# Kernel optimization log

Hardware: AMD Instinct MI355X
Metric: run time of the kernel (lower is better)

The kernel has to match this reference:

```python
import jax, jax.numpy as jnp
import numpy as np
import math

D_MODEL = 1024
N_HEADS = 16
HEAD_DIM = D_MODEL // N_HEADS
B, T = 2, 2048


def _rope(q, k):
    # q, k: (B, H, T, Dh)
    Dh = q.shape[-1]
    Tq = q.shape[2]
    dim = jnp.arange(0, Dh, 2, dtype=jnp.float32)
    inv_freq = 1.0 / (10000.0 ** (dim / Dh))
    pos = jnp.arange(Tq, dtype=jnp.float32)
    freqs = pos[:, None] * inv_freq[None, :]          # (T, Dh/2)
    sin = jnp.sin(freqs)[None, None]                  # (1,1,T,Dh/2)
    cos = jnp.cos(freqs)[None, None]

    def rot(t):
        te, to = t[..., ::2], t[..., 1::2]
        re = te * cos - to * sin
        ro = te * sin + to * cos
        return jnp.stack([re, ro], axis=-1).reshape(t.shape)

    return rot(q), rot(k)


def setup_inputs() -> dict:
    key = jax.random.key(0)
    ks = jax.random.split(key, 4)
    std = 1.0 / math.sqrt(D_MODEL)
    x = jax.random.normal(ks[0], (B, T, D_MODEL), dtype=jnp.float32)
    W_qkv = jax.random.normal(ks[1], (D_MODEL, 3 * D_MODEL), dtype=jnp.float32) * std
    b_qkv = jnp.zeros((3 * D_MODEL,), dtype=jnp.float32)
    W_out = jax.random.normal(ks[2], (D_MODEL, D_MODEL), dtype=jnp.float32) * std
    b_out = jnp.zeros((D_MODEL,), dtype=jnp.float32)
    attention_mask = jnp.ones((B, T), dtype=jnp.int32)
    return {"x": x, "attention_mask": attention_mask, "W_qkv": W_qkv,
            "b_qkv": b_qkv, "W_out": W_out, "b_out": b_out}


def reference(x, attention_mask, W_qkv, b_qkv, W_out, b_out):
    Bx, Tx, D = x.shape
    qkv = x @ W_qkv + b_qkv                            # (B,T,3D)
    q, k, v = jnp.split(qkv, 3, axis=-1)
    # (B,T,H,Dh) -> (B,H,T,Dh)
    q = q.reshape(Bx, Tx, N_HEADS, HEAD_DIM).transpose(0, 2, 1, 3)
    k = k.reshape(Bx, Tx, N_HEADS, HEAD_DIM).transpose(0, 2, 1, 3)
    v = v.reshape(Bx, Tx, N_HEADS, HEAD_DIM).transpose(0, 2, 1, 3)
    q, k = _rope(q, k)
    scale = 1.0 / math.sqrt(float(HEAD_DIM))
    scores = jnp.einsum('bhqd,bhkd->bhqk', q, k) * scale
    causal = jnp.tril(jnp.ones((Tx, Tx), dtype=bool))[None, None]
    pad = attention_mask.astype(bool)[:, None, None, :]
    mask = causal & pad
    scores = jnp.where(mask, scores, -jnp.inf)
    probs = jax.nn.softmax(scores, axis=-1)
    out = jnp.einsum('bhqk,bhkd->bhqd', probs, v)      # (B,H,T,Dh)
    out = out.transpose(0, 2, 1, 3).reshape(Bx, Tx, D)
    return out @ W_out + b_out
```

## Files before the change

kernel.cpp:

```cpp
#include <hip/hip_runtime.h>
#include <math.h>
#include <stdint.h>

#define D_MODEL 1024
#define N_HEADS 16
#define HEAD_DIM 64
#define BATCH 2
#define SEQ 2048
#define TOKENS (BATCH * SEQ)

typedef __attribute__((ext_vector_type(8))) short short8;
typedef __attribute__((ext_vector_type(8))) _Float16 half8;
typedef __attribute__((ext_vector_type(4))) float floatx4;

#define BMFMA(a, b, c) __builtin_amdgcn_mfma_f32_16x16x32_bf16(a, b, c, 0, 0, 0)
#define HMFMA(a, b, c) __builtin_amdgcn_mfma_f32_16x16x32_f16(a, b, c, 0, 0, 0)

__device__ __forceinline__ unsigned short f2bf(float f) {
    uint32_t u = __float_as_uint(f);
    u += 0x7fffu + ((u >> 16) & 1u);
    return (unsigned short)(u >> 16);
}
__device__ __forceinline__ float bf2f(unsigned short h) {
    return __uint_as_float(((uint32_t)h) << 16);
}
__device__ __forceinline__ unsigned short f2h(float f) {
    union { _Float16 h; unsigned short u; } cv;
    cv.h = (_Float16)f;
    return cv.u;
}
__device__ __forceinline__ float h2f(unsigned short u) {
    union { unsigned short u; _Float16 h; } cv;
    cv.u = u;
    return (float)cv.h;
}
__device__ __forceinline__ void ld16h(const unsigned short* p, float* f) {
    uint4 u0 = *(const uint4*)p;
    uint4 u1 = *(const uint4*)(p + 8);
    const uint32_t* a = (const uint32_t*)&u0;
    const uint32_t* b = (const uint32_t*)&u1;
#pragma unroll
    for (int j = 0; j < 4; ++j) {
        f[2 * j]     = h2f((unsigned short)(a[j] & 0xffffu));
        f[2 * j + 1] = h2f((unsigned short)(a[j] >> 16));
        f[8 + 2 * j]     = h2f((unsigned short)(b[j] & 0xffffu));
        f[8 + 2 * j + 1] = h2f((unsigned short)(b[j] >> 16));
    }
}

#define GLD_LDS16(gp, lp) __builtin_amdgcn_global_load_lds(                 \
    (const __attribute__((address_space(1))) void*)(gp),                    \
    (__attribute__((address_space(3))) void*)(lp), 16, 0, 0)

__global__ __launch_bounds__(256) void split_inputs(
    const float* __restrict__ X, const float* __restrict__ Wqkv,
    const float* __restrict__ Wout, const int* __restrict__ am,
    unsigned short* __restrict__ Axh, unsigned short* __restrict__ Bt,
    unsigned short* __restrict__ Bt2, unsigned long long* __restrict__ mbits,
    float2* __restrict__ tab)
{
    __shared__ float t[32][33];
    const int tid = threadIdx.x;
    const int bid = blockIdx.x;
    if (bid < 2048) {
        const int idx = bid * 2048 + tid * 8;
        const int row = idx >> 10;
        const int c = idx & 1023;
        float4 v0 = *(const float4*)(X + (size_t)row * 1024 + c);
        float4 v1 = *(const float4*)(X + (size_t)row * 1024 + c + 4);
        float f[8] = {v0.x, v0.y, v0.z, v0.w, v1.x, v1.y, v1.z, v1.w};
        uint32_t p[4];
#pragma unroll
        for (int j = 0; j < 4; ++j)
            p[j] = (uint32_t)f2h(f[2 * j]) | ((uint32_t)f2h(f[2 * j + 1]) << 16);
        *(uint4*)(Axh + (size_t)row * 1024 + c) = *(uint4*)p;
    } else if (bid < 5120) {
        const int id = bid - 2048;
        const int n0 = (id % 96) * 32, k0 = (id / 96) * 32;
        const int c = tid & 31, r = tid >> 5;
#pragma unroll
        for (int i = 0; i < 4; ++i)
            t[r + 8 * i][c] = Wqkv[(size_t)(k0 + r + 8 * i) * 3072 + n0 + c];
        __syncthreads();
#pragma unroll
        for (int i = 0; i < 4; ++i) {
            int dn = r + 8 * i;
            Bt[(size_t)(n0 + dn) * 1024 + k0 + c] = f2h(t[c][dn]);
        }
    } else if (bid < 6144) {
        const int id = bid - 5120;
        const int n0 = (id & 31) * 32, k0 = (id >> 5) * 32;
        const int c = tid & 31, r = tid >> 5;
#pragma unroll
        for (int i = 0; i < 4; ++i)
            t[r + 8 * i][c] = Wout[(size_t)(k0 + r + 8 * i) * 1024 + n0 + c];
        __syncthreads();
#pragma unroll
        for (int i = 0; i < 4; ++i) {
            int dn = r + 8 * i;
            Bt2[(size_t)(n0 + dn) * 1024 + k0 + c] = f2h(t[c][dn]);
        }
    } else if (bid == 6144) {
        if (tid < 64) {
            const int* a = am + tid * 64;
            unsigned long long m = 0ull;
            for (int j = 0; j < 64; ++j)
                m |= (unsigned long long)(a[j] != 0 ? 1u : 0u) << j;
            mbits[tid] = m;
        }
    } else {
        const int i = bid - 6145;
#pragma unroll
        for (int e = 0; e < 16; ++e) {
            int idx = i * 4096 + e * 256 + tid;
            int tt = idx >> 5, pr = idx & 31;
            double ex = (double)(2 * pr) / 64.0;
            float inv = (float)exp2(-ex * 13.287712379549449);
            float ang = (float)tt * inv;
            float s, c;
            __sincosf(ang, &s, &c);
            tab[idx] = make_float2(c, s);
        }
    }
}

template<int WM, int WN, int FM, int FN, int OUT16>
__global__ __launch_bounds__(256) void gemm_mfma_h(
    const unsigned short* __restrict__ A, int lda,
    const unsigned short* __restrict__ Bt, int ldb,
    const float* __restrict__ bias, void* __restrict__ Cv, int ldc, int nTiles)
{
    constexpr int BM = WM * FM * 16;
    constexpr int BN = WN * FN * 16;
    constexpr int NA = BM / 64;
    constexpr int NB = BN / 64;

    __shared__ __align__(16) unsigned short sA0[BM * 32];
    __shared__ __align__(16) unsigned short sA1[BM * 32];
    __shared__ __align__(16) unsigned short sB0[BN * 32];
    __shared__ __align__(16) unsigned short sB1[BN * 32];

    const int tid = threadIdx.x;
    const int w = tid >> 6, lane = tid & 63;
    const int l15 = lane & 15, quad = lane >> 4;
    const int wm = w / WN, wn = w % WN;

    const int lin = blockIdx.x;
    const int msuper = lin / (8 * nTiles);
    const int rem = lin % (8 * nTiles);
    const int m0 = (msuper * 8 + (rem & 7)) * BM;
    const int n0 = (rem >> 3) * BN;

    const int ch = (lane & 3) ^ ((lane >> 3) & 3);
    const int sw = (quad ^ ((l15 >> 1) & 3)) * 8;

    const unsigned short* aG[NA];
    const unsigned short* bG[NB];
#pragma unroll
    for (int i = 0; i < NA; ++i)
        aG[i] = A + (size_t)(m0 + (w * NA + i) * 16 + (lane >> 2)) * lda + ch * 8;
#pragma unroll
    for (int i = 0; i < NB; ++i)
        bG[i] = Bt + (size_t)(n0 + (w * NB + i) * 16 + (lane >> 2)) * ldb + ch * 8;

    floatx4 acc[FM][FN];
#pragma unroll
    for (int fm = 0; fm < FM; ++fm)
#pragma unroll
        for (int fn = 0; fn < FN; ++fn) acc[fm][fn] = (floatx4)0.f;

    for (int ks = 0; ks < 16; ++ks) {
        const int ko = ks * 64;
        __syncthreads();
#pragma unroll
        for (int i = 0; i < NA; ++i) {
            GLD_LDS16(aG[i] + ko,      sA0 + (w * NA + i) * 512);
            GLD_LDS16(aG[i] + ko + 32, sA1 + (w * NA + i) * 512);
        }
#pragma unroll
        for (int i = 0; i < NB; ++i) {
            GLD_LDS16(bG[i] + ko,      sB0 + (w * NB + i) * 512);
            GLD_LDS16(bG[i] + ko + 32, sB1 + (w * NB + i) * 512);
        }
        __syncthreads();

        half8 a0[FM], a1[FM], b0[FN], b1[FN];
#pragma unroll
        for (int fm = 0; fm < FM; ++fm) {
            const int off = ((wm * FM + fm) * 16 + l15) * 32 + sw;
            a0[fm] = *(const half8*)&sA0[off];
            a1[fm] = *(const half8*)&sA1[off];
        }
#pragma unroll
        for (int fn = 0; fn < FN; ++fn) {
            const int off = ((wn * FN + fn) * 16 + l15) * 32 + sw;
            b0[fn] = *(const half8*)&sB0[off];
            b1[fn] = *(const half8*)&sB1[off];
        }
#pragma unroll
        for (int fm = 0; fm < FM; ++fm)
#pragma unroll
            for (int fn = 0; fn < FN; ++fn) {
                floatx4 a = acc[fm][fn];
                a = HMFMA(a0[fm], b0[fn], a);
                a = HMFMA(a1[fm], b1[fn], a);
                acc[fm][fn] = a;
            }
    }

#pragma unroll
    for (int fm = 0; fm < FM; ++fm)
#pragma unroll
        for (int fn = 0; fn < FN; ++fn) {
            int col = n0 + (wn * FN + fn) * 16 + l15;
            float bv = bias[col];
#pragma unroll
            for (int r = 0; r < 4; ++r) {
                int row = m0 + (wm * FM + fm) * 16 + quad * 4 + r;
                if (OUT16) {
                    ((unsigned short*)Cv)[(size_t)row * ldc + col] =
                        f2h(acc[fm][fn][r] + bv);
                } else {
                    ((float*)Cv)[(size_t)row * ldc + col] =
                        acc[fm][fn][r] + bv;
                }
            }
        }
}

__global__ __launch_bounds__(256) void prep_qkv(
    const unsigned short* __restrict__ qkvh, const float2* __restrict__ tab,
    unsigned short* __restrict__ Qh, unsigned short* __restrict__ Kh,
    unsigned short* __restrict__ Vh)
{
    __shared__ float vt[64][65];
    const int tid = threadIdx.x;
    const int lin = blockIdx.x;
    const int tt = lin & 31, bh = lin >> 5;
    const int b = bh >> 4, h = bh & 15;
    const int r = tid >> 2;
    const int dblk = (tid & 3) * 16;
    const int tg = tt * 64 + r;
    const size_t src = (size_t)(b * SEQ + tg) * 3072 + h * 64 + dblk;
    const size_t dst = ((size_t)bh * SEQ + tg) * 64 + dblk;

    float q[16], k[16], v[16];
    ld16h(qkvh + src, q);
    ld16h(qkvh + src + 1024, k);
    ld16h(qkvh + src + 2048, v);

    float2 cs[8];
#pragma unroll
    for (int i = 0; i < 4; ++i)
        *(float4*)&cs[2 * i] = *(const float4*)(tab + (size_t)tg * 32
                                                + (dblk >> 1) + 2 * i);
#pragma unroll
    for (int j = 0; j < 16; j += 2) {
        float c = cs[j >> 1].x, s = cs[j >> 1].y;
        float qe = q[j], qo = q[j + 1];
        q[j] = qe * c - qo * s; q[j + 1] = qe * s + qo * c;
        float ke = k[j], ko = k[j + 1];
        k[j] = ke * c - ko * s; k[j + 1] = ke * s + ko * c;
    }
    uint32_t ph[8];
#pragma unroll
    for (int j = 0; j < 8; ++j) {
        float f0 = q[2 * j] * 0.125f, f1 = q[2 * j + 1] * 0.125f;
        ph[j] = (uint32_t)f2h(f0) | ((uint32_t)f2h(f1) << 16);
    }
    *(uint4*)(Qh + dst) = *(uint4*)&ph[0]; *(uint4*)(Qh + dst + 8) = *(uint4*)&ph[4];
#pragma unroll
    for (int j = 0; j < 8; ++j)
        ph[j] = (uint32_t)f2h(k[2 * j]) | ((uint32_t)f2h(k[2 * j + 1]) << 16);
    *(uint4*)(Kh + dst) = *(uint4*)&ph[0]; *(uint4*)(Kh + dst + 8) = *(uint4*)&ph[4];

#pragma unroll
    for (int j = 0; j < 16; ++j) vt[r][dblk + j] = v[j];
    __syncthreads();
    const int d2 = tid >> 2;
    const int tb = (tid & 3) * 16;
#pragma unroll
    for (int j = 0; j < 8; ++j) {
        float f0 = vt[tb + 2 * j][d2], f1 = vt[tb + 2 * j + 1][d2];
        ph[j] = (uint32_t)f2bf(f0) | ((uint32_t)f2bf(f1) << 16);
    }
    const size_t vdst = ((size_t)bh * 64 + d2) * SEQ + tt * 64 + tb;
    *(uint4*)(Vh + vdst) = *(uint4*)&ph[0]; *(uint4*)(Vh + vdst + 8) = *(uint4*)&ph[4];
}

__global__ __launch_bounds__(256, 4) void flash_mfma(
    const unsigned short* __restrict__ Qh, const unsigned short* __restrict__ Kh,
    const unsigned short* __restrict__ Vh,
    const unsigned long long* __restrict__ mbits,
    unsigned short* __restrict__ attnx)
{
    __shared__ __align__(16) unsigned short sK[4096];
    __shared__ __align__(16) unsigned short sV[4096];
    __shared__ __align__(16) unsigned short sP[4096];

    const int tid = threadIdx.x;
    const int lane = tid & 63, w = tid >> 6;
    const int l15 = lane & 15, quad = lane >> 4;
    const int lin0 = blockIdx.x;
    const int xcd = lin0 & 7, idx = lin0 >> 3;
    const int g = idx >> 2, j = idx & 3;
    const int bh = xcd * 4 + j;
    const int qt = (j & 1) ? (31 - g) : g;
    const int b = bh >> 4, h = bh & 15;
    const int sw = (quad ^ ((l15 >> 1) & 3)) * 8;
    const int ch = (lane & 3) ^ ((lane >> 3) & 3);
    unsigned short* pbase = sP + w * 1024;

    short8 ones;
#pragma unroll
    for (int jj = 0; jj < 8; ++jj) ones[jj] = (short)0x3F80;

    const size_t qb = ((size_t)bh * SEQ + qt * 64 + w * 16 + l15) * 64 + quad * 8;
    const half8 qh0 = *(const half8*)(Qh + qb);
    const half8 qh1 = *(const half8*)(Qh + qb + 32);

    unsigned int mlo = 0xffffffffu, mhi = 0xffffffffu;
    if (lane < 32) {
        unsigned long long mw = mbits[b * 32 + lane];
        mlo = (unsigned int)mw;
        mhi = (unsigned int)(mw >> 32);
    }
    const bool fullmask =
        (__ballot((mlo & mhi) == 0xffffffffu) == ~0ull);

    const size_t kRow0 = ((size_t)bh * SEQ + w * 16 + (lane >> 2)) * 64 + ch * 8;
    const size_t vRow  = ((size_t)bh * 64 + w * 16 + (lane >> 2)) * SEQ + ch * 8;

    floatx4 O[4];
    floatx4 lAcc = (floatx4)0.f;
#pragma unroll
    for (int nf = 0; nf < 4; ++nf) O[nf] = (floatx4)0.f;

    const int mg = qt * 64 + w * 16 + l15;

    for (int kt = 0; kt <= qt; ++kt) {
        __syncthreads();
        {
            const size_t kg = kRow0 + (size_t)kt * 64 * 64;
            const size_t vg = vRow + kt * 64;
            GLD_LDS16(Kh + kg,      sK + w * 512);
            GLD_LDS16(Kh + kg + 32, sK + 2048 + w * 512);
            GLD_LDS16(Vh + vg,      sV + w * 512);
            GLD_LDS16(Vh + vg + 32, sV + 2048 + w * 512);
        }
        __syncthreads();

        const bool diag = (kt == qt);
        unsigned int wlo = 0xffffffffu, whi = 0xffffffffu;
        if (!fullmask) {
            wlo = (unsigned int)__shfl((int)mlo, kt);
            whi = (unsigned int)__shfl((int)mhi, kt);
        }

#pragma unroll
        for (int nf = 0; nf < 4; ++nf) {
            const int base = (nf * 16 + l15) * 32 + sw;
            const half8 k0 = *(const half8*)&sK[base];
            const half8 k1 = *(const half8*)&sK[2048 + base];
            floatx4 s = (floatx4)0.f;
            s = HMFMA(k0, qh0, s);
            s = HMFMA(k1, qh1, s);

            float pv[4];
            if (fullmask && !diag) {
#pragma unroll
                for (int r = 0; r < 4; ++r)
                    pv[r] = __expf(s[r] - 16.0f);
            } else {
                const int tb = kt * 64 + nf * 16 + quad * 4;
                const unsigned int msel = (nf & 2) ? whi : wlo;
                const int p4 = (nf & 1) * 16 + quad * 4;
#pragma unroll
                for (int r = 0; r < 4; ++r) {
                    bool ok = ((msel >> (p4 + r)) & 1u) != 0u;
                    if (diag) ok = ok && (tb + r <= mg);
                    pv[r] = ok ? __expf(s[r] - 16.0f) : 0.0f;
                }
            }
            uint32_t w0, w1;
            asm("v_cvt_pk_bf16_f32 %0, %1, %2" : "=v"(w0) : "v"(pv[0]), "v"(pv[1]));
            asm("v_cvt_pk_bf16_f32 %0, %1, %2" : "=v"(w1) : "v"(pv[2]), "v"(pv[3]));
            const int pos = (((nf & 1) * 2 + (quad >> 1)) ^ ((l15 >> 1) & 3));
            *(uint2*)(pbase + (nf >> 1) * 512 + l15 * 32 + pos * 8
                      + (quad & 1) * 4) = make_uint2(w0, w1);
        }

        const short8 pf0 = *(const short8*)(pbase + l15 * 32 + sw);
        const short8 pf1 = *(const short8*)(pbase + 512 + l15 * 32 + sw);

        lAcc = BMFMA(pf0, ones, lAcc);
        lAcc = BMFMA(pf1, ones, lAcc);
#pragma unroll
        for (int nf = 0; nf < 4; ++nf) {
            const int vb = (nf * 16 + l15) * 32 + sw;
            floatx4 o = O[nf];
            o = BMFMA(pf0, *(const short8*)&sV[vb], o);
            o = BMFMA(pf1, *(const short8*)&sV[2048 + vb], o);
            O[nf] = o;
        }
    }

    float rl[4];
#pragma unroll
    for (int r = 0; r < 4; ++r) rl[r] = 1.0f / lAcc[r];
#pragma unroll
    for (int nf = 0; nf < 4; ++nf)
#pragma unroll
        for (int r = 0; r < 4; ++r) {
            const int tok = b * SEQ + qt * 64 + w * 16 + quad * 4 + r;
            const int col = h * 64 + nf * 16 + l15;
            attnx[(size_t)tok * 1024 + col] = f2h(O[nf][r] * rl[r]);
        }
}

extern "C" void kernel_launch(void* const* d_in, const int* in_sizes, int n_in,
                              void* d_out, int out_size, void* d_ws, size_t ws_size,
                              hipStream_t stream)
{
    const float* x    = (const float*)d_in[0];
    const int*   am   = (const int*)d_in[1];
    const float* Wqkv = (const float*)d_in[2];
    const float* bqkv = (const float*)d_in[3];
    const float* Wout = (const float*)d_in[4];
    const float* bout = (const float*)d_in[5];
    float* out = (float*)d_out;

    char* ws = (char*)d_ws;
    unsigned short* Bt  = (unsigned short*)ws;
    unsigned short* Bt2 = (unsigned short*)(ws + 6291456);
    float2* tab = (float2*)(ws + 8388608);
    unsigned long long* mbits = (unsigned long long*)(ws + 8912896);
    unsigned short* qkvh = (unsigned short*)(ws + 12582912);
    unsigned short* attnx = qkvh;
    unsigned short* Qh = (unsigned short*)(ws + 62914560);
    unsigned short* Kh = (unsigned short*)(ws + 71303168);
    unsigned short* Vh = (unsigned short*)(ws + 79691776);
    unsigned short* Axh = (unsigned short*)(ws + 88080384);

    split_inputs<<<6161, 256, 0, stream>>>(x, Wqkv, Wout, am,
                                           Axh, Bt, Bt2, mbits, tab);

    gemm_mfma_h<2, 2, 4, 4, 1><<<768, 256, 0, stream>>>(
        Axh, 1024, Bt, 1024, bqkv, qkvh, 3072, 24);

    prep_qkv<<<1024, 256, 0, stream>>>(qkvh, tab, Qh, Kh, Vh);

    flash_mfma<<<1024, 256, 0, stream>>>(Qh, Kh, Vh, mbits, attnx);

    gemm_mfma_h<2, 2, 4, 4, 0><<<256, 256, 0, stream>>>(
        attnx, 1024, Bt2, 1024, bout, out, 1024, 8);
}
```

Measured before the change: 193.4 us.

## Split long causal query tiles across two blocks and merge partial outputs

Query tiles 16-31 now have their key range split into two halves, each handled by its own block that writes unnormalized partial O and row sums to workspace. A new merge kernel adds the two partials, normalizes, and writes fp16 output. Short tiles still run in a single block with direct output. The aim is to balance work across 1536 blocks instead of a causal triangle with long tail blocks. The cost is an extra launch and fp32 partial traffic. The merge is valid only because softmax uses a fixed max offset of 16, so partial sums add directly. Launch bounds are also raised to 6 waves.

```diff
diff --git a/kernel.cpp b/kernel.cpp
--- a/kernel.cpp
+++ b/kernel.cpp
@@ -288,11 +288,12 @@
     *(uint4*)(Vh + vdst) = *(uint4*)&ph[0]; *(uint4*)(Vh + vdst + 8) = *(uint4*)&ph[4];
 }
 
-__global__ __launch_bounds__(256, 4) void flash_mfma(
+__global__ __launch_bounds__(256, 6) void flash_mfma(
     const unsigned short* __restrict__ Qh, const unsigned short* __restrict__ Kh,
     const unsigned short* __restrict__ Vh,
     const unsigned long long* __restrict__ mbits,
-    unsigned short* __restrict__ attnx)
+    unsigned short* __restrict__ attnx,
+    float* __restrict__ Opart, float* __restrict__ lpart)
 {
     __shared__ __align__(16) unsigned short sK[4096];
     __shared__ __align__(16) unsigned short sV[4096];
@@ -303,9 +304,15 @@
     const int l15 = lane & 15, quad = lane >> 4;
     const int lin0 = blockIdx.x;
     const int xcd = lin0 & 7, idx = lin0 >> 3;
-    const int g = idx >> 2, j = idx & 3;
-    const int bh = xcd * 4 + j;
-    const int qt = (j & 1) ? (31 - g) : g;
+    const int bh = xcd * 4 + (idx & 3);
+    const int rank = idx >> 2;
+    int qt, k0, kend, mode;
+    if (rank < 16)        { qt = 16 + rank; k0 = 0;  kend = 15; mode = 1; }
+    else {
+        const int i = (rank - 16) >> 1;
+        if ((rank & 1) == 0) { qt = 31 - i; k0 = 16; kend = qt; mode = 2; }
+        else                 { qt = 15 - i; k0 = 0;  kend = qt; mode = 0; }
+    }
     const int b = bh >> 4, h = bh & 15;
     const int sw = (quad ^ ((l15 >> 1) & 3)) * 8;
     const int ch = (lane & 3) ^ ((lane >> 3) & 3);
@@ -338,11 +345,11 @@
 
     const int mg = qt * 64 + w * 16 + l15;
 
-    for (int kt = 0; kt <= qt; ++kt) {
+    for (int kt = k0; kt <= kend; ++kt) {
         __syncthreads();
         {
             const size_t kg = kRow0 + (size_t)kt * 64 * 64;
-            const size_t vg = vRow + kt * 64;
+            const size_t vg = vRow + (size_t)kt * 64;
             GLD_LDS16(Kh + kg,      sK + w * 512);
             GLD_LDS16(Kh + kg + 32, sK + 2048 + w * 512);
             GLD_LDS16(Vh + vg,      sV + w * 512);
@@ -360,11 +367,11 @@
 #pragma unroll
         for (int nf = 0; nf < 4; ++nf) {
             const int base = (nf * 16 + l15) * 32 + sw;
-            const half8 k0 = *(const half8*)&sK[base];
-            const half8 k1 = *(const half8*)&sK[2048 + base];
+            const half8 k0v = *(const half8*)&sK[base];
+            const half8 k1v = *(const half8*)&sK[2048 + base];
             floatx4 s = (floatx4)0.f;
-            s = HMFMA(k0, qh0, s);
-            s = HMFMA(k1, qh1, s);
+            s = HMFMA(k0v, qh0, s);
+            s = HMFMA(k1v, qh1, s);
 
             float pv[4];
             if (fullmask && !diag) {
@@ -405,17 +412,63 @@
         }
     }
 
-    float rl[4];
-#pragma unroll
-    for (int r = 0; r < 4; ++r) rl[r] = 1.0f / lAcc[r];
-#pragma unroll
-    for (int nf = 0; nf < 4; ++nf)
-#pragma unroll
-        for (int r = 0; r < 4; ++r) {
-            const int tok = b * SEQ + qt * 64 + w * 16 + quad * 4 + r;
-            const int col = h * 64 + nf * 16 + l15;
-            attnx[(size_t)tok * 1024 + col] = f2h(O[nf][r] * rl[r]);
-        }
+    if (mode == 0) {
+        float rl[4];
+#pragma unroll
+        for (int r = 0; r < 4; ++r) rl[r] = 1.0f / lAcc[r];
+#pragma unroll
+        for (int nf = 0; nf < 4; ++nf)
+#pragma unroll
+            for (int r = 0; r < 4; ++r) {
+                const int tok = b * SEQ + qt * 64 + w * 16 + quad * 4 + r;
+                const int col = h * 64 + nf * 16 + l15;
+                attnx[(size_t)tok * 1024 + col] = f2h(O[nf][r] * rl[r]);
+            }
+    } else {
+        const int qt16 = qt - 16;
+        float* Op = Opart + ((mode == 2) ? 2097152 : 0)
+                  + (((size_t)bh * 16 + qt16) * 64) * 64;
+#pragma unroll
+        for (int nf = 0; nf < 4; ++nf)
+#pragma unroll
+            for (int r = 0; r < 4; ++r)
+                Op[(w * 16 + quad * 4 + r) * 64 + nf * 16 + l15] = O[nf][r];
+        if (l15 == 0) {
+            float* lp = lpart + ((mode == 2) ? 32768 : 0)
+                      + (bh * 16 + qt16) * 64;
+#pragma unroll
+            for (int r = 0; r < 4; ++r)
+                lp[w * 16 + quad * 4 + r] = lAcc[r];
+        }
+    }
+}
+
+__global__ __launch_bounds__(256) void flash_merge(
+    const float* __restrict__ Opart, const float* __restrict__ lpart,
+    unsigned short* __restrict__ attnx)
+{
+    const int bh = blockIdx.x >> 4, qt16 = blockIdx.x & 15;
+    const int b = bh >> 4, h = bh & 15;
+    const int tid = threadIdx.x;
+    const int q = tid >> 2, dblk = (tid & 3) * 16;
+    const size_t ob = (((size_t)bh * 16 + qt16) * 64 + q) * 64 + dblk;
+    const int lb = (bh * 16 + qt16) * 64 + q;
+    const float rl = 1.0f / (lpart[lb] + lpart[lb + 32768]);
+
+    uint32_t ph[8];
+#pragma unroll
+    for (int i = 0; i < 4; ++i) {
+        float4 a = *(const float4*)(Opart + ob + 4 * i);
+        float4 c = *(const float4*)(Opart + ob + 2097152 + 4 * i);
+        float f0 = (a.x + c.x) * rl, f1 = (a.y + c.y) * rl;
+        float f2 = (a.z + c.z) * rl, f3 = (a.w + c.w) * rl;
+        ph[2 * i]     = (uint32_t)f2h(f0) | ((uint32_t)f2h(f1) << 16);
+        ph[2 * i + 1] = (uint32_t)f2h(f2) | ((uint32_t)f2h(f3) << 16);
+    }
+    const int tok = b * SEQ + (16 + qt16) * 64 + q;
+    unsigned short* dst = attnx + (size_t)tok * 1024 + h * 64 + dblk;
+    *(uint4*)dst = *(uint4*)&ph[0];
+    *(uint4*)(dst + 8) = *(uint4*)&ph[4];
 }
 
 extern "C" void kernel_launch(void* const* d_in, const int* in_sizes, int n_in,
@@ -441,6 +494,8 @@
     unsigned short* Kh = (unsigned short*)(ws + 71303168);
     unsigned short* Vh = (unsigned short*)(ws + 79691776);
     unsigned short* Axh = (unsigned short*)(ws + 88080384);
+    float* Opart = (float*)(ws + 88080384);
+    float* lpart = (float*)(ws + 104857600);
 
     split_inputs<<<6161, 256, 0, stream>>>(x, Wqkv, Wout, am,
                                            Axh, Bt, Bt2, mbits, tab);
@@ -450,7 +505,9 @@
 
     prep_qkv<<<1024, 256, 0, stream>>>(qkvh, tab, Qh, Kh, Vh);
 
-    flash_mfma<<<1024, 256, 0, stream>>>(Qh, Kh, Vh, mbits, attnx);
+    flash_mfma<<<1536, 256, 0, stream>>>(Qh, Kh, Vh, mbits, attnx,
+                                         Opart, lpart);
+    flash_merge<<<512, 256, 0, stream>>>(Opart, lpart, attnx);
 
     gemm_mfma_h<2, 2, 4, 4, 0><<<256, 256, 0, stream>>>(
         attnx, 1024, Bt2, 1024, bout, out, 1024, 8);
```

New measurement: 192.2 us. No clear change (-0.6%).
